# Optimization experiments

Measured on AMD Instinct MI355X. Metric: run time of the kernel, lower is better.

## Reference

```python
import jax, jax.numpy as jnp
import numpy as np

N, D = 128, 512  # batch, hypercube dim (in_features == n_2d_layers == out_features)

def setup_inputs() -> dict:
    key = jax.random.key(0)
    k1, k2, k3 = jax.random.split(key, 3)
    bound = 1.0 / np.sqrt(D)
    x = jax.random.normal(k1, (N, D, D), dtype=jnp.float32)
    # kaiming_uniform_(a=sqrt(5)) on (in, layers, out) ~ U(-1/sqrt(fan_in), 1/sqrt(fan_in)) scale
    w = jax.random.uniform(k2, (D, D, D), dtype=jnp.float32, minval=-bound, maxval=bound)
    b = jax.random.uniform(k3, (D, D), dtype=jnp.float32, minval=-bound, maxval=bound)
    return {"x": x, "w": w, "b": b}

def reference(x, w, b):
    # Original: (x.expand((L, *x.shape)).movedim(0,-2) * w).sum(-1) + b
    # which reduces to out[n,i,j] = sum_k x[n,i,k] * w[i,j,k] + b[i,j]
    # (w axes: (in_features, n_2d_layers, out_features), all equal D)
    return jnp.einsum('nik,ijk->nij', x, w) + b
```

## Files before the change

kernel.cpp:

```cpp
#include <hip/hip_runtime.h>


#define Dd 512
#define DD (512 * 512)

typedef __attribute__((ext_vector_type(8))) short bf16x8;
typedef __attribute__((ext_vector_type(4))) short bf16x4;
typedef __attribute__((ext_vector_type(4))) float f32x4;

__device__ __forceinline__ short f2bf(float f) {
    unsigned u = __builtin_bit_cast(unsigned, f);
    u += 0x7FFFu + ((u >> 16) & 1u);
    return (short)(u >> 16);
}

__device__ __forceinline__ bf16x8 cvt8(float4 a, float4 b) {
    bf16x8 h;
    h[0] = f2bf(a.x); h[1] = f2bf(a.y); h[2] = f2bf(a.z); h[3] = f2bf(a.w);
    h[4] = f2bf(b.x); h[5] = f2bf(b.y); h[6] = f2bf(b.z); h[7] = f2bf(b.w);
    return h;
}

__device__ __forceinline__ void glds16(const float* g, float* l) {
    __builtin_amdgcn_global_load_lds(
        (const __attribute__((address_space(1))) void*)g,
        (__attribute__((address_space(3))) void*)l, 16, 0, 0);
}

__global__ __launch_bounds__(512, 4)
void linear3d_kernel(const float* __restrict__ x,
                     const float* __restrict__ w,
                     const float* __restrict__ b,
                     float* __restrict__ out) {
    const int i    = blockIdx.x;
    const int tid  = threadIdx.x;
    const int lane = tid & 63;
    const int wid  = tid >> 6;
    const int row16 = lane & 15;
    const int cg    = lane >> 4;
    const int sw    = (row16 & 7) << 4;

    __shared__ float f32r[2][8192];

    const float* xi = x + (size_t)i * Dd;
    const float* wi = w + (size_t)i * DD;

#define WGLDS(cidx, slot) do {                                                 \
    const float* gsrc_ = wi + (size_t)(cidx) * 8192;                           \
    _Pragma("unroll")                                                          \
    for (int q = 0; q < 4; ++q) {                                              \
        int t_ = wid * 4 + q; int row_ = t_ >> 1;                              \
        int off_ = (((t_ & 1) * 1024) + lane * 16) ^ ((row_ & 7) << 4);        \
        glds16(gsrc_ + row_ * 512 + (off_ >> 2), &f32r[slot][t_ * 256]);       \
    }                                                                          \
} while (0)

    WGLDS(0, 0);

    short* xs = (short*)&f32r[1][0];
    bf16x8 xf[16];
    for (int r = 0; r < 8; ++r) {
        __syncthreads();
        #pragma unroll
        for (int p = 0; p < 4; ++p) {
            int idx4 = tid + p * 512;
            int row = idx4 >> 7, c4 = idx4 & 127;
            float4 v = *(const float4*)(xi + (size_t)(r * 16 + row) * DD + c4 * 4);
            bf16x4 h = { f2bf(v.x), f2bf(v.y), f2bf(v.z), f2bf(v.w) };
            int byte = (row * 1024 + c4 * 8) ^ ((row & 7) << 4);
            *(bf16x4*)((char*)xs + byte) = h;
        }
        __syncthreads();
        if (wid == r) {
            #pragma unroll
            for (int s = 0; s < 16; ++s) {
                int byte = (row16 * 1024 + s * 64 + cg * 16) ^ sw;
                xf[s] = *(const bf16x8*)((const char*)xs + byte);
            }
        }
    }
    __syncthreads();

    WGLDS(1, 1);
    float bias_cur = b[i * Dd + row16];

#define BODY(c, VMSTR, DO_GLDS, DO_BIAS, DO_SYNC) do {                         \
    float biasN_ = bias_cur;                                                   \
    if (DO_BIAS) biasN_ = b[i * Dd + ((c) + 1) * 16 + row16];                  \
    const float* buf_ = &f32r[(c) & 1][0] + row16 * 512;                       \
    const int K0_ = ((cg * 32) ^ sw) >> 2;                                     \
    const int K1_ = ((cg * 32) ^ sw ^ 16) >> 2;                                \
    f32x4 accA = {0.f, 0.f, 0.f, 0.f}, accB = {0.f, 0.f, 0.f, 0.f};            \
    _Pragma("unroll")                                                          \
    for (int s = 0; s < 16; s += 2) {                                          \
        float4 a0_ = *(const float4*)(buf_ + K0_ + s * 32);                    \
        float4 a1_ = *(const float4*)(buf_ + K1_ + s * 32);                    \
        float4 b0_ = *(const float4*)(buf_ + K0_ + (s + 1) * 32);              \
        float4 b1_ = *(const float4*)(buf_ + K1_ + (s + 1) * 32);              \
        accA = __builtin_amdgcn_mfma_f32_16x16x32_bf16(                        \
            xf[s], cvt8(a0_, a1_), accA, 0, 0, 0);                             \
        accB = __builtin_amdgcn_mfma_f32_16x16x32_bf16(                        \
            xf[s + 1], cvt8(b0_, b1_), accB, 0, 0, 0);                         \
    }                                                                          \
    { int j_ = (c) * 16 + row16;                                               \
      _Pragma("unroll")                                                        \
      for (int r_ = 0; r_ < 4; ++r_) {                                         \
          int n_ = wid * 16 + cg * 4 + r_;                                     \
          out[(size_t)n_ * DD + (size_t)i * Dd + j_] =                         \
              accA[r_] + accB[r_] + bias_cur;                                  \
      } }                                                                      \
    bias_cur = biasN_;                                                         \
    if (DO_SYNC) {                                                             \
        asm volatile("s_waitcnt " VMSTR ::: "memory");                         \
        __builtin_amdgcn_s_barrier();                                          \
        __builtin_amdgcn_sched_barrier(0);                                     \
    }                                                                          \
    if (DO_GLDS) {                                                             \
        WGLDS((c) + 2, (c) & 1);                                               \
        __builtin_amdgcn_sched_barrier(0);                                     \
    }                                                                          \
} while (0)

    BODY(0, "vmcnt(5)", true, true, true);
    #pragma unroll 1
    for (int c = 1; c <= 29; ++c)
        BODY(c, "vmcnt(5)", true, true, true);
    BODY(30, "vmcnt(5)", false, true, true);
    BODY(31, "vmcnt(0)", false, false, false);

#undef BODY
#undef WGLDS
}

extern "C" void kernel_launch(void* const* d_in, const int* in_sizes, int n_in,
                              void* d_out, int out_size, void* d_ws, size_t ws_size,
                              hipStream_t stream) {
    const float* x = (const float*)d_in[0];
    const float* w = (const float*)d_in[1];
    const float* b = (const float*)d_in[2];
    float* out = (float*)d_out;
    linear3d_kernel<<<dim3(Dd), dim3(512), 0, stream>>>(x, w, b, out);
}
```

Baseline: 190.1 us.

## Convert weight tiles to bf16 once in LDS with triple-buffered half-chunk pipeline

The weight staging is restructured into half-chunks of 16 rows by 256 k, loaded into three fp32 LDS slots. Each half-chunk is converted to bf16 once into a double-buffered bf16 LDS area, instead of every wave reconverting all fp32 weights itself. Bias moves into LDS, and the prefetch now runs three stages deep. This removes redundant per-wave fp32-to-bf16 conversion and halves LDS read bytes per MFMA, at the cost of twice as many barriers, an extra LDS write/read pass, and more delicate vmcnt accounting.

```diff
diff --git a/kernel.cpp b/kernel.cpp
--- a/kernel.cpp
+++ b/kernel.cpp
@@ -12,13 +12,6 @@
     unsigned u = __builtin_bit_cast(unsigned, f);
     u += 0x7FFFu + ((u >> 16) & 1u);
     return (short)(u >> 16);
-}
-
-__device__ __forceinline__ bf16x8 cvt8(float4 a, float4 b) {
-    bf16x8 h;
-    h[0] = f2bf(a.x); h[1] = f2bf(a.y); h[2] = f2bf(a.z); h[3] = f2bf(a.w);
-    h[4] = f2bf(b.x); h[5] = f2bf(b.y); h[6] = f2bf(b.z); h[7] = f2bf(b.w);
-    return h;
 }
 
 __device__ __forceinline__ void glds16(const float* g, float* l) {
@@ -38,26 +31,40 @@
     const int wid  = tid >> 6;
     const int row16 = lane & 15;
     const int cg    = lane >> 4;
-    const int sw    = (row16 & 7) << 4;
 
-    __shared__ float f32r[2][8192];
+    __shared__ float f32r[3][4096];
+    __shared__ short bfb[2][4096];
+    __shared__ float ldsb[Dd];
 
     const float* xi = x + (size_t)i * Dd;
     const float* wi = w + (size_t)i * DD;
 
-#define WGLDS(cidx, slot) do {                                                 \
-    const float* gsrc_ = wi + (size_t)(cidx) * 8192;                           \
+    ldsb[tid] = b[i * Dd + tid];
+
+#define GLDS(H, SLOT) do {                                                     \
+    int p_ = (H) >> 1, kh_ = (H) & 1;                                          \
     _Pragma("unroll")                                                          \
-    for (int q = 0; q < 4; ++q) {                                              \
-        int t_ = wid * 4 + q; int row_ = t_ >> 1;                              \
-        int off_ = (((t_ & 1) * 1024) + lane * 16) ^ ((row_ & 7) << 4);        \
-        glds16(gsrc_ + row_ * 512 + (off_ >> 2), &f32r[slot][t_ * 256]);       \
+    for (int q = 0; q < 2; ++q) {                                              \
+        int jr_ = 2 * wid + q;                                                 \
+        glds16(wi + (size_t)(p_ * 16 + jr_) * 512 + kh_ * 256 + lane * 4,      \
+               &f32r[SLOT][jr_ * 256]);                                        \
     }                                                                          \
 } while (0)
 
-    WGLDS(0, 0);
+#define CONV(SLOT, BUF) do {                                                   \
+    _Pragma("unroll")                                                          \
+    for (int q = 0; q < 2; ++q) {                                              \
+        int jr_ = 2 * wid + q;                                                 \
+        float4 v_ = *(const float4*)(&f32r[SLOT][jr_ * 256 + lane * 4]);       \
+        bf16x4 h_ = { f2bf(v_.x), f2bf(v_.y), f2bf(v_.z), f2bf(v_.w) };        \
+        int byte_ = jr_ * 512 + ((lane * 8) ^ ((jr_ & 7) << 4));               \
+        *(bf16x4*)((char*)&bfb[BUF][0] + byte_) = h_;                          \
+    }                                                                          \
+} while (0)
 
-    short* xs = (short*)&f32r[1][0];
+    GLDS(0, 0); GLDS(1, 1); GLDS(2, 2);
+
+    short* xs = &bfb[0][0];
     bf16x8 xf[16];
     for (int r = 0; r < 8; ++r) {
         __syncthreads();
@@ -74,62 +81,71 @@
         if (wid == r) {
             #pragma unroll
             for (int s = 0; s < 16; ++s) {
-                int byte = (row16 * 1024 + s * 64 + cg * 16) ^ sw;
+                int byte = (row16 * 1024 + s * 64 + cg * 16) ^ ((row16 & 7) << 4);
                 xf[s] = *(const bf16x8*)((const char*)xs + byte);
             }
         }
     }
     __syncthreads();
 
-    WGLDS(1, 1);
-    float bias_cur = b[i * Dd + row16];
+    CONV(0, 0);
+    asm volatile("s_waitcnt lgkmcnt(0)" ::: "memory");
+    __builtin_amdgcn_s_barrier();
+    __builtin_amdgcn_sched_barrier(0);
 
-#define BODY(c, VMSTR, DO_GLDS, DO_BIAS, DO_SYNC) do {                         \
-    float biasN_ = bias_cur;                                                   \
-    if (DO_BIAS) biasN_ = b[i * Dd + ((c) + 1) * 16 + row16];                  \
-    const float* buf_ = &f32r[(c) & 1][0] + row16 * 512;                       \
-    const int K0_ = ((cg * 32) ^ sw) >> 2;                                     \
-    const int K1_ = ((cg * 32) ^ sw ^ 16) >> 2;                                \
-    f32x4 accA = {0.f, 0.f, 0.f, 0.f}, accB = {0.f, 0.f, 0.f, 0.f};            \
+    f32x4 accA = {0.f, 0.f, 0.f, 0.f}, accB = {0.f, 0.f, 0.f, 0.f};
+
+#define BODY(H, SG, SC, PAR, VMSTR, DO_GLDS, DO_WC) do {                       \
+    if (DO_GLDS) GLDS((H) + 3, SG);                                            \
     _Pragma("unroll")                                                          \
-    for (int s = 0; s < 16; s += 2) {                                          \
-        float4 a0_ = *(const float4*)(buf_ + K0_ + s * 32);                    \
-        float4 a1_ = *(const float4*)(buf_ + K1_ + s * 32);                    \
-        float4 b0_ = *(const float4*)(buf_ + K0_ + (s + 1) * 32);              \
-        float4 b1_ = *(const float4*)(buf_ + K1_ + (s + 1) * 32);              \
-        accA = __builtin_amdgcn_mfma_f32_16x16x32_bf16(                        \
-            xf[s], cvt8(a0_, a1_), accA, 0, 0, 0);                             \
-        accB = __builtin_amdgcn_mfma_f32_16x16x32_bf16(                        \
-            xf[s + 1], cvt8(b0_, b1_), accB, 0, 0, 0);                         \
+    for (int s = 0; s < 8; s += 2) {                                           \
+        int byA_ = row16 * 512 + ((s * 64 + cg * 16) ^ ((row16 & 7) << 4));    \
+        int byB_ = row16 * 512 + (((s + 1) * 64 + cg * 16) ^ ((row16 & 7) << 4)); \
+        bf16x8 wfA_ = *(const bf16x8*)((const char*)&bfb[PAR][0] + byA_);      \
+        bf16x8 wfB_ = *(const bf16x8*)((const char*)&bfb[PAR][0] + byB_);      \
+        accA = __builtin_amdgcn_mfma_f32_16x16x32_bf16(xf[(PAR)*8 + s], wfA_, accA, 0, 0, 0);     \
+        accB = __builtin_amdgcn_mfma_f32_16x16x32_bf16(xf[(PAR)*8 + s + 1], wfB_, accB, 0, 0, 0); \
     }                                                                          \
-    { int j_ = (c) * 16 + row16;                                               \
-      _Pragma("unroll")                                                        \
-      for (int r_ = 0; r_ < 4; ++r_) {                                         \
-          int n_ = wid * 16 + cg * 4 + r_;                                     \
-          out[(size_t)n_ * DD + (size_t)i * Dd + j_] =                         \
-              accA[r_] + accB[r_] + bias_cur;                                  \
-      } }                                                                      \
-    bias_cur = biasN_;                                                         \
-    if (DO_SYNC) {                                                             \
+    if (PAR) {                                                                 \
+        int j_ = ((H) >> 1) * 16 + row16;                                      \
+        float bias_ = ldsb[j_];                                                \
+        _Pragma("unroll")                                                      \
+        for (int r_ = 0; r_ < 4; ++r_) {                                       \
+            int n_ = wid * 16 + cg * 4 + r_;                                   \
+            out[(size_t)n_ * DD + (size_t)i * Dd + j_] =                       \
+                accA[r_] + accB[r_] + bias_;                                   \
+        }                                                                      \
+        accA = (f32x4){0.f, 0.f, 0.f, 0.f};                                    \
+        accB = (f32x4){0.f, 0.f, 0.f, 0.f};                                    \
+    }                                                                          \
+    if (DO_WC) {                                                               \
         asm volatile("s_waitcnt " VMSTR ::: "memory");                         \
+        __builtin_amdgcn_sched_barrier(0);                                     \
+        CONV(SC, (PAR) ^ 1);                                                   \
+        asm volatile("s_waitcnt lgkmcnt(0)" ::: "memory");                     \
         __builtin_amdgcn_s_barrier();                                          \
-        __builtin_amdgcn_sched_barrier(0);                                     \
-    }                                                                          \
-    if (DO_GLDS) {                                                             \
-        WGLDS((c) + 2, (c) & 1);                                               \
         __builtin_amdgcn_sched_barrier(0);                                     \
     }                                                                          \
 } while (0)
 
-    BODY(0, "vmcnt(5)", true, true, true);
     #pragma unroll 1
-    for (int c = 1; c <= 29; ++c)
-        BODY(c, "vmcnt(5)", true, true, true);
-    BODY(30, "vmcnt(5)", false, true, true);
-    BODY(31, "vmcnt(0)", false, false, false);
+    for (int u = 0; u < 10; ++u) {
+        int h = 6 * u;
+        BODY(h + 0, 0, 1, 0, "vmcnt(8)",  true, true);
+        BODY(h + 1, 1, 2, 1, "vmcnt(12)", true, true);
+        BODY(h + 2, 2, 0, 0, "vmcnt(8)",  true, true);
+        BODY(h + 3, 0, 1, 1, "vmcnt(12)", true, true);
+        BODY(h + 4, 1, 2, 0, "vmcnt(8)",  true, true);
+        BODY(h + 5, 2, 0, 1, "vmcnt(12)", true, true);
+    }
+    BODY(60, 0, 1, 0, "vmcnt(8)",  true,  true);
+    BODY(61, 1, 2, 1, "vmcnt(10)", false, true);
+    BODY(62, 2, 0, 0, "vmcnt(4)",  false, true);
+    BODY(63, 0, 1, 1, "vmcnt(0)",  false, false);
 
 #undef BODY
-#undef WGLDS
+#undef CONV
+#undef GLDS
 }
 
 extern "C" void kernel_launch(void* const* d_in, const int* in_sizes, int n_in,
```

Result: slower. 232.9 us (+22.5%).
